# Kernel optimization log

Measured on AMD Instinct MI355X. Metric: run time of the kernel, lower is better.

## Reference

```python
import jax, jax.numpy as jnp
import numpy as np

NUM_EXPERTS = 8
HIDDEN = 1024
TOKENS = 8192


def setup_inputs() -> dict:
    key = jax.random.key(0)
    k1, k2, k3, k4 = jax.random.split(key, 4)
    inp = jax.random.normal(k1, (TOKENS, HIDDEN), dtype=jnp.float32)
    gate = jax.random.normal(k2, (TOKENS, NUM_EXPERTS), dtype=jnp.float32)
    # expert parameters: one dense layer per expert (H -> H)
    W = jax.random.normal(k3, (NUM_EXPERTS, HIDDEN, HIDDEN), dtype=jnp.float32) / np.sqrt(HIDDEN)
    b = jax.random.normal(k4, (NUM_EXPERTS, HIDDEN), dtype=jnp.float32) * 0.01
    return {"input": inp, "gate": gate, "W": W, "b": b}


def reference(input, gate, W, b):
    # Routing: softmax over router logits, top-1 expert per token.
    probs = jax.nn.softmax(gate, axis=-1)            # [T, E]
    expert_idx = jnp.argmax(probs, axis=-1)          # [T]
    top_p = jnp.take_along_axis(probs, expert_idx[:, None], axis=-1)[:, 0]  # [T]

    # Dispatch + grouped GEMM (computed densely for all experts, then masked):
    # y[e, t, d] = input[t, :] @ W[e] + b[e]
    y = jnp.einsum("th,ehd->etd", input, W) + b[:, None, :]  # [E, T, H]

    # Combine: select the routed expert's output, scaled by its gate prob.
    dispatch = jax.nn.one_hot(expert_idx, NUM_EXPERTS, dtype=input.dtype) * top_p[:, None]  # [T, E]
    out = jnp.einsum("etd,te->td", y, dispatch)      # [T, H]
    return out
```

## Files before the change

### kernel.cpp

```cpp
#include <hip/hip_runtime.h>
#include <hip/hip_bf16.h>
#include <cstdint>
#include <cstddef>

#define TOK 8192
#define HID 1024
#define NE 8

typedef __bf16 bf16x4 __attribute__((ext_vector_type(4)));
typedef __bf16 bf16x8 __attribute__((ext_vector_type(8)));
typedef float floatx4 __attribute__((ext_vector_type(4)));

static __device__ __forceinline__ __bf16 f2bf(float x) {
    unsigned u = __builtin_bit_cast(unsigned, x);
    u += 0x7fffu + ((u >> 16) & 1u);
    unsigned short hs = (unsigned short)(u >> 16);
    return __builtin_bit_cast(__bf16, hs);
}

__global__ void route_kernel(const float* __restrict__ gate, float* __restrict__ scale,
                             int* __restrict__ counts, int* __restrict__ list) {
    __shared__ int hcnt[NE];
    __shared__ int hbase[NE];
    const int t = threadIdx.x;
    if (t < NE) hcnt[t] = 0;
    __syncthreads();
    int tok = blockIdx.x * 256 + t;
    float g[NE];
#pragma unroll
    for (int j = 0; j < NE; j++) g[j] = gate[tok * NE + j];
    float gm = g[0]; int best = 0;
#pragma unroll
    for (int j = 1; j < NE; j++) {
        if (g[j] > gm) { gm = g[j]; best = j; }
    }
    float s = 0.f;
#pragma unroll
    for (int j = 0; j < NE; j++) s += __expf(g[j] - gm);
    scale[tok] = 1.0f / s;
    int lpos = atomicAdd(&hcnt[best], 1);
    __syncthreads();
    if (t < NE) hbase[t] = atomicAdd(&counts[t], hcnt[t]);
    __syncthreads();
    list[best * TOK + hbase[best] + lpos] = tok;
}

__global__ void prep_kernel(const float* __restrict__ X, const float* __restrict__ W,
                            const int* __restrict__ counts, const int* __restrict__ list,
                            __bf16* __restrict__ Xg, __bf16* __restrict__ Wf) {
    const int b = blockIdx.x;
    const int t = threadIdx.x;

    if (b < 8192) {
        const int e  = b >> 10;
        const int rem = b & 1023;
        const int sg = rem >> 2;
        const int kq = rem & 3;
        const int cnt = counts[e];
        const int aligned = (cnt + 127) & ~127;
        if (sg * 32 >= aligned) return;

        int xb = 0;
#pragma unroll
        for (int j = 0; j < NE; j++) if (j < e) xb += (counts[j] + 127) & ~127;
        const int xb16 = xb >> 4;

        const int wave = t >> 6, lane = t & 63;
        const int ln = lane & 15, q = lane >> 4;
        const int ngl = wave & 1;
        const int slot = sg * 32 + ngl * 16 + ln;
        const bool v = (slot < cnt);
        const int tk = v ? list[e * TOK + slot] : 0;
        const float* rp = X + (size_t)tk * HID + q * 8;
        __bf16* dst = Xg + ((size_t)(xb16 + sg * 2 + ngl) * 32) * 512 + lane * 8;

#pragma unroll
        for (int c = 0; c < 4; c++) {
            const int kc = kq * 8 + (wave >> 1) * 4 + c;
            float4 x0 = make_float4(0.f, 0.f, 0.f, 0.f), x1 = x0;
            if (v) {
                x0 = *(const float4*)(rp + kc * 32);
                x1 = *(const float4*)(rp + kc * 32 + 4);
            }
            bf16x8 o;
            o[0] = f2bf(x0.x); o[1] = f2bf(x0.y); o[2] = f2bf(x0.z); o[3] = f2bf(x0.w);
            o[4] = f2bf(x1.x); o[5] = f2bf(x1.y); o[6] = f2bf(x1.z); o[7] = f2bf(x1.w);
            *(bf16x8*)(dst + (size_t)kc * 512) = o;
        }
    } else {
        const int bb = b - 8192;
        const int e  = bb >> 8;
        const int kt = (bb >> 4) & 15;
        const int nt = bb & 15;
        const int k0 = kt * 64, n0 = nt * 64;

        __shared__ float ld[64][65];
        {
            const int r4 = t >> 4, c4 = t & 15;
#pragma unroll
            for (int i = 0; i < 4; i++) {
                int kl = r4 + 16 * i;
                float4 v = *(const float4*)(W + ((size_t)e * HID + (k0 + kl)) * HID + n0 + c4 * 4);
                ld[kl][c4 * 4 + 0] = v.x; ld[kl][c4 * 4 + 1] = v.y;
                ld[kl][c4 * 4 + 2] = v.z; ld[kl][c4 * 4 + 3] = v.w;
            }
        }
        __syncthreads();
        const int wave = t >> 6, lane = t & 63;
        const int ln = lane & 15, q = lane >> 4;
#pragma unroll
        for (int rep = 0; rep < 2; rep++) {
            const int fb = rep * 4 + wave;
            const int ngl = fb & 3;
            const int kcl = fb >> 2;
            const int n = ngl * 16 + ln;
            bf16x8 o;
#pragma unroll
            for (int j = 0; j < 8; j++) o[j] = f2bf(ld[kcl * 32 + q * 8 + j][n]);
            const size_t grp = (size_t)(e * 64 + nt * 4 + ngl);
            *(bf16x8*)(Wf + (grp * 32 + kt * 2 + kcl) * 512 + lane * 8) = o;
        }
    }
}

__launch_bounds__(256)
__global__ void moe_gemm_bf16(const __bf16* __restrict__ Xg, const __bf16* __restrict__ Wf,
                              const float* __restrict__ Bias, const float* __restrict__ scale,
                              const int* __restrict__ counts, const int* __restrict__ list,
                              float* __restrict__ out) {
    const int bid = blockIdx.x;
    const int e  = bid & 7;
    const int mt = (bid >> 3) & 63;
    const int nt = bid >> 9;

    const int cnt = counts[e];
    if (mt * 128 >= cnt) return;
    const int n0 = nt * 128;

    int xb = 0;
#pragma unroll
    for (int j = 0; j < NE; j++) if (j < e) xb += (counts[j] + 127) & ~127;
    const int xb16 = xb >> 4;

    const int tid  = threadIdx.x;
    const int lane = tid & 63;
    const int wave = tid >> 6;
    const int ln = lane & 15;
    const int q  = lane >> 4;
    const int wm = (wave >> 1) * 64;
    const int wn = (wave & 1) * 64;

    const __bf16* aBase[4];
    const __bf16* bBase[4];
#pragma unroll
    for (int i = 0; i < 4; i++) {
        const size_t mgrp = (size_t)(xb16 + mt * 8 + (wm >> 4) + i);
        aBase[i] = Xg + mgrp * 16384 + lane * 8;
        const size_t ngrp = (size_t)(e * 64 + nt * 8 + (wn >> 4) + i);
        bBase[i] = Wf + ngrp * 16384 + lane * 8;
    }

    floatx4 acc[4][4];
#pragma unroll
    for (int mi = 0; mi < 4; mi++)
#pragma unroll
        for (int ni = 0; ni < 4; ni++) acc[mi][ni] = (floatx4){0.f, 0.f, 0.f, 0.f};

    bf16x8 af[3][4], bf[3][4];
#pragma unroll
    for (int s = 0; s < 2; s++)
#pragma unroll
        for (int i = 0; i < 4; i++) {
            af[s][i] = *(const bf16x8*)(aBase[i] + s * 512);
            bf[s][i] = *(const bf16x8*)(bBase[i] + s * 512);
        }

#pragma unroll
    for (int kc = 0; kc < 32; kc++) {
        const int cur = kc % 3;
        if (kc + 2 < 32) {
            const int nxt = (kc + 2) % 3;
#pragma unroll
            for (int i = 0; i < 4; i++) {
                af[nxt][i] = *(const bf16x8*)(aBase[i] + (kc + 2) * 512);
                bf[nxt][i] = *(const bf16x8*)(bBase[i] + (kc + 2) * 512);
            }
        }
#pragma unroll
        for (int mi = 0; mi < 4; mi++)
#pragma unroll
            for (int ni = 0; ni < 4; ni++)
                acc[mi][ni] = __builtin_amdgcn_mfma_f32_16x16x32_bf16(
                    af[cur][mi], bf[cur][ni], acc[mi][ni], 0, 0, 0);
    }

    float bn[4];
#pragma unroll
    for (int ni = 0; ni < 4; ni++) bn[ni] = Bias[e * HID + n0 + wn + ni * 16 + ln];

#pragma unroll
    for (int mi = 0; mi < 4; mi++) {
#pragma unroll
        for (int r = 0; r < 4; r++) {
            const int slot = mt * 128 + wm + mi * 16 + q * 4 + r;
            if (slot < cnt) {
                const int tk = list[e * TOK + slot];
                const float sc = scale[tk];
                const size_t ob = (size_t)tk * HID + n0 + wn + ln;
#pragma unroll
                for (int ni = 0; ni < 4; ni++)
                    __builtin_nontemporal_store(sc * (acc[mi][ni][r] + bn[ni]),
                                                &out[ob + ni * 16]);
            }
        }
    }
}

__launch_bounds__(256)
__global__ void moe_gemm_fb(const float* __restrict__ X, const float* __restrict__ W,
                            const float* __restrict__ Bias, const float* __restrict__ scale,
                            const int* __restrict__ counts, const int* __restrict__ list,
                            float* __restrict__ out) {
    const int bid = blockIdx.x;
    const int e  = bid >> 9;
    const int nt = (bid >> 6) & 7;
    const int mt = bid & 63;
    const int cnt = counts[e];
    if (mt * 128 >= cnt) return;
    const int mvalid = min(128, cnt - mt * 128);
    const int n0 = nt * 128;

    __shared__ __bf16 As[128 * 64];
    __shared__ __bf16 Bs[128 * 64];
    __shared__ int   tok[128];
    __shared__ float scl[128];

    const int tid = threadIdx.x;
    if (tid < 128) {
        int g = mt * 128 + tid;
        int tk = (g < cnt) ? list[e * TOK + g] : 0;
        tok[tid] = tk;
        scl[tid] = (g < cnt) ? scale[tk] : 0.f;
    }
    __syncthreads();

    const int c4 = tid & 15;
    const float* rp[8];
    bool rv[8];
#pragma unroll
    for (int i = 0; i < 8; i++) {
        int m = (tid >> 4) + 16 * i;
        rv[i] = (m < mvalid);
        rp[i] = X + (size_t)tok[m] * HID;
    }
    const int n4 = tid & 31;
    const int kb = tid >> 5;
    const float* wbase = W + (size_t)e * HID * HID + (size_t)(kb * 8) * HID + n0 + n4 * 4;

    const int lane = tid & 63;
    const int ln = lane & 15;
    const int q  = lane >> 4;
    const int wave = tid >> 6;
    const int wm = (wave >> 1) * 64;
    const int wn = (wave & 1) * 64;

    floatx4 acc[4][4];
#pragma unroll
    for (int mi = 0; mi < 4; mi++)
#pragma unroll
        for (int ni = 0; ni < 4; ni++) acc[mi][ni] = (floatx4){0.f, 0.f, 0.f, 0.f};

    for (int k0 = 0; k0 < HID; k0 += 64) {
#pragma unroll
        for (int i = 0; i < 8; i++) {
            int m = (tid >> 4) + 16 * i;
            float4 v = make_float4(0.f, 0.f, 0.f, 0.f);
            if (rv[i]) v = *(const float4*)(rp[i] + k0 + c4 * 4);
            bf16x4 b4;
            b4[0] = f2bf(v.x); b4[1] = f2bf(v.y); b4[2] = f2bf(v.z); b4[3] = f2bf(v.w);
            int chunk = c4 >> 1;
            int addr = m * 64 + ((chunk ^ (m & 7)) * 8) + (c4 & 1) * 4;
            *(bf16x4*)(&As[addr]) = b4;
        }
        {
            const float* wp = wbase + (size_t)k0 * HID;
            float4 rr[8];
#pragma unroll
            for (int r = 0; r < 8; r++) rr[r] = *(const float4*)(wp + (size_t)r * HID);
#pragma unroll
            for (int j = 0; j < 4; j++) {
                int n = n4 * 4 + j;
                int c = kb ^ (n & 7);
                bf16x8 pk;
                pk[0] = f2bf(j == 0 ? rr[0].x : j == 1 ? rr[0].y : j == 2 ? rr[0].z : rr[0].w);
                pk[1] = f2bf(j == 0 ? rr[1].x : j == 1 ? rr[1].y : j == 2 ? rr[1].z : rr[1].w);
                pk[2] = f2bf(j == 0 ? rr[2].x : j == 1 ? rr[2].y : j == 2 ? rr[2].z : rr[2].w);
                pk[3] = f2bf(j == 0 ? rr[3].x : j == 1 ? rr[3].y : j == 2 ? rr[3].z : rr[3].w);
                pk[4] = f2bf(j == 0 ? rr[4].x : j == 1 ? rr[4].y : j == 2 ? rr[4].z : rr[4].w);
                pk[5] = f2bf(j == 0 ? rr[5].x : j == 1 ? rr[5].y : j == 2 ? rr[5].z : rr[5].w);
                pk[6] = f2bf(j == 0 ? rr[6].x : j == 1 ? rr[6].y : j == 2 ? rr[6].z : rr[6].w);
                pk[7] = f2bf(j == 0 ? rr[7].x : j == 1 ? rr[7].y : j == 2 ? rr[7].z : rr[7].w);
                *(bf16x8*)(&Bs[n * 64 + c * 8]) = pk;
            }
        }
        __syncthreads();
#pragma unroll
        for (int kk = 0; kk < 64; kk += 32) {
            const int cbase = (kk >> 3) + q;
            bf16x8 af[4], bfv[4];
#pragma unroll
            for (int mi = 0; mi < 4; mi++) {
                int row = wm + mi * 16 + ln;
                af[mi] = *(const bf16x8*)(&As[row * 64 + ((cbase ^ (row & 7)) * 8)]);
            }
#pragma unroll
            for (int ni = 0; ni < 4; ni++) {
                int n = wn + ni * 16 + ln;
                bfv[ni] = *(const bf16x8*)(&Bs[n * 64 + ((cbase ^ (n & 7)) * 8)]);
            }
#pragma unroll
            for (int mi = 0; mi < 4; mi++)
#pragma unroll
                for (int ni = 0; ni < 4; ni++)
                    acc[mi][ni] = __builtin_amdgcn_mfma_f32_16x16x32_bf16(
                        af[mi], bfv[ni], acc[mi][ni], 0, 0, 0);
        }
        __syncthreads();
    }

    float bn[4];
#pragma unroll
    for (int ni = 0; ni < 4; ni++) bn[ni] = Bias[e * HID + n0 + wn + ni * 16 + ln];
#pragma unroll
    for (int mi = 0; mi < 4; mi++) {
#pragma unroll
        for (int r = 0; r < 4; r++) {
            int row = wm + mi * 16 + q * 4 + r;
            if (row < mvalid) {
                int t = tok[row];
                float sc = scl[row];
                size_t ob = (size_t)t * HID + n0 + wn + ln;
#pragma unroll
                for (int ni = 0; ni < 4; ni++)
                    out[ob + ni * 16] = sc * (acc[mi][ni][r] + bn[ni]);
            }
        }
    }
}

extern "C" void kernel_launch(void* const* d_in, const int* in_sizes, int n_in,
                              void* d_out, int out_size, void* d_ws, size_t ws_size,
                              hipStream_t stream) {
    const float* X    = (const float*)d_in[0];
    const float* G    = (const float*)d_in[1];
    const float* W    = (const float*)d_in[2];
    const float* Bias = (const float*)d_in[3];
    float* out = (float*)d_out;

    float* scale = (float*)d_ws;
    int* counts  = (int*)((char*)d_ws + 32768);
    int* list    = (int*)((char*)d_ws + 36864);
    __bf16* Xg   = (__bf16*)((char*)d_ws + 299008);
    __bf16* Wf   = (__bf16*)((char*)d_ws + 299008 + 18874368);
    const size_t need = 299008 + 18874368 + 16777216ULL;

    hipMemsetAsync(counts, 0, NE * sizeof(int), stream);

    if (ws_size >= need) {
        route_kernel<<<TOK / 256, 256, 0, stream>>>(G, scale, counts, list);
        prep_kernel<<<10240, 256, 0, stream>>>(X, W, counts, list, Xg, Wf);
        moe_gemm_bf16<<<8 * 64 * 8, 256, 0, stream>>>(Xg, Wf, Bias, scale, counts, list, out);
    } else {
        route_kernel<<<TOK / 256, 256, 0, stream>>>(G, scale, counts, list);
        moe_gemm_fb<<<NE * 64 * 8, 256, 0, stream>>>(X, W, Bias, scale, counts, list, out);
    }
}
```

Before: 175.9 us.

## Stage GEMM tiles through double-buffered LDS via direct global-to-LDS loads

The grouped GEMM kernel used to load its A and B fragments straight from global memory into registers, so each wave fetched its own copies and paired waves re-read the same data. It now loads each 128x64 K-slab of X and W into double-buffered shared memory with global_load_lds, sharing the data across the four waves. MFMA operands are then read from LDS, and the next slab is prefetched during compute. This cuts redundant global and L2 traffic and register pressure, at the cost of a __syncthreads per K-step, 64KB of LDS that limits occupancy, and a shallower prefetch than the previous 3-stage register pipeline.

```diff
diff --git a/kernel.cpp b/kernel.cpp
--- a/kernel.cpp
+++ b/kernel.cpp
@@ -140,60 +140,78 @@
     int xb = 0;
 #pragma unroll
     for (int j = 0; j < NE; j++) if (j < e) xb += (counts[j] + 127) & ~127;
-    const int xb16 = xb >> 4;
+    const int mgrpb = (xb >> 4) + mt * 8;
+    const int ngrpb = e * 64 + nt * 8;
+
+    __shared__ __bf16 As[2][8192];
+    __shared__ __bf16 Bs[2][8192];
 
     const int tid  = threadIdx.x;
     const int lane = tid & 63;
     const int wave = tid >> 6;
     const int ln = lane & 15;
     const int q  = lane >> 4;
+
+    const __bf16* asrc[4];
+    const __bf16* bsrc[4];
+#pragma unroll
+    for (int c = 0; c < 4; c++) {
+        const int gi  = wave * 2 + (c >> 1);
+        const int kcl = c & 1;
+        asrc[c] = Xg + (size_t)(mgrpb + gi) * 16384 + kcl * 512 + lane * 8;
+        bsrc[c] = Wf + (size_t)(ngrpb + gi) * 16384 + kcl * 512 + lane * 8;
+    }
+
+    auto stage = [&](int kt, int buf) {
+        const int koff = kt * 1024;
+#pragma unroll
+        for (int c = 0; c < 4; c++) {
+            __builtin_amdgcn_global_load_lds(
+                (const __attribute__((address_space(1))) void*)(asrc[c] + koff),
+                (__attribute__((address_space(3))) void*)(&As[buf][(wave * 4 + c) * 512]),
+                16, 0, 0);
+            __builtin_amdgcn_global_load_lds(
+                (const __attribute__((address_space(1))) void*)(bsrc[c] + koff),
+                (__attribute__((address_space(3))) void*)(&Bs[buf][(wave * 4 + c) * 512]),
+                16, 0, 0);
+        }
+    };
+
+    floatx4 acc[4][4];
+#pragma unroll
+    for (int mi = 0; mi < 4; mi++)
+#pragma unroll
+        for (int ni = 0; ni < 4; ni++) acc[mi][ni] = (floatx4){0.f, 0.f, 0.f, 0.f};
+
+    const int wmg = (wave >> 1) * 4;
+    const int wng = (wave & 1) * 4;
+
+    stage(0, 0);
+    for (int kt = 0; kt < 16; ++kt) {
+        __syncthreads();
+        if (kt < 15) stage(kt + 1, (kt + 1) & 1);
+        const int buf = kt & 1;
+
+#pragma unroll
+        for (int kcl = 0; kcl < 2; kcl++) {
+            bf16x8 af[4], bfv[4];
+#pragma unroll
+            for (int mi = 0; mi < 4; mi++)
+                af[mi] = *(const bf16x8*)(&As[buf][((wmg + mi) * 2 + kcl) * 512 + lane * 8]);
+#pragma unroll
+            for (int ni = 0; ni < 4; ni++)
+                bfv[ni] = *(const bf16x8*)(&Bs[buf][((wng + ni) * 2 + kcl) * 512 + lane * 8]);
+#pragma unroll
+            for (int mi = 0; mi < 4; mi++)
+#pragma unroll
+                for (int ni = 0; ni < 4; ni++)
+                    acc[mi][ni] = __builtin_amdgcn_mfma_f32_16x16x32_bf16(
+                        af[mi], bfv[ni], acc[mi][ni], 0, 0, 0);
+        }
+    }
+
     const int wm = (wave >> 1) * 64;
     const int wn = (wave & 1) * 64;
-
-    const __bf16* aBase[4];
-    const __bf16* bBase[4];
-#pragma unroll
-    for (int i = 0; i < 4; i++) {
-        const size_t mgrp = (size_t)(xb16 + mt * 8 + (wm >> 4) + i);
-        aBase[i] = Xg + mgrp * 16384 + lane * 8;
-        const size_t ngrp = (size_t)(e * 64 + nt * 8 + (wn >> 4) + i);
-        bBase[i] = Wf + ngrp * 16384 + lane * 8;
-    }
-
-    floatx4 acc[4][4];
-#pragma unroll
-    for (int mi = 0; mi < 4; mi++)
-#pragma unroll
-        for (int ni = 0; ni < 4; ni++) acc[mi][ni] = (floatx4){0.f, 0.f, 0.f, 0.f};
-
-    bf16x8 af[3][4], bf[3][4];
-#pragma unroll
-    for (int s = 0; s < 2; s++)
-#pragma unroll
-        for (int i = 0; i < 4; i++) {
-            af[s][i] = *(const bf16x8*)(aBase[i] + s * 512);
-            bf[s][i] = *(const bf16x8*)(bBase[i] + s * 512);
-        }
-
-#pragma unroll
-    for (int kc = 0; kc < 32; kc++) {
-        const int cur = kc % 3;
-        if (kc + 2 < 32) {
-            const int nxt = (kc + 2) % 3;
-#pragma unroll
-            for (int i = 0; i < 4; i++) {
-                af[nxt][i] = *(const bf16x8*)(aBase[i] + (kc + 2) * 512);
-                bf[nxt][i] = *(const bf16x8*)(bBase[i] + (kc + 2) * 512);
-            }
-        }
-#pragma unroll
-        for (int mi = 0; mi < 4; mi++)
-#pragma unroll
-            for (int ni = 0; ni < 4; ni++)
-                acc[mi][ni] = __builtin_amdgcn_mfma_f32_16x16x32_bf16(
-                    af[cur][mi], bf[cur][ni], acc[mi][ni], 0, 0, 0);
-    }
-
     float bn[4];
 #pragma unroll
     for (int ni = 0; ni < 4; ni++) bn[ni] = Bias[e * HID + n0 + wn + ni * 16 + ln];
```

New measurement: 162.7 us. 7.5% less time.
